# Kernel tuning notes

Measured on AMD Instinct MI355X. Metric: run time of the kernel, lower is better.

Reference implementation:

```python
import jax, jax.numpy as jnp
import numpy as np

B, S, D = 4, 2048, 1024
H, HD = 16, 64  # n_head, head_dim; H*HD == D

def setup_inputs() -> dict:
    key = jax.random.key(0)
    k1, k2, k3 = jax.random.split(key, 3)
    x = jax.random.normal(k1, (B, S, D), dtype=jnp.float32)
    # nn.Linear weights: stored [out, in]; init ~ U(-1/sqrt(in), 1/sqrt(in))
    w_attn = jax.random.uniform(k2, (3 * D, D), dtype=jnp.float32,
                                minval=-1.0, maxval=1.0) / jnp.sqrt(jnp.float32(D))
    w_proj = jax.random.uniform(k3, (D, D), dtype=jnp.float32,
                                minval=-1.0, maxval=1.0) / jnp.sqrt(jnp.float32(D))
    return {"x": x, "w_attn": w_attn, "w_proj": w_proj}

def reference(x, w_attn, w_proj):
    b, s, d = x.shape
    qkv = jnp.einsum('bsd,ed->bse', x, w_attn)              # [b, s, 3D]
    q, k, v = jnp.split(qkv, 3, axis=-1)
    q = q.reshape(b, s, H, HD).transpose(0, 2, 1, 3)        # [b, h, s, hd]
    k = k.reshape(b, s, H, HD).transpose(0, 2, 1, 3)
    v = v.reshape(b, s, H, HD).transpose(0, 2, 1, 3)
    scale = 1.0 / jnp.sqrt(jnp.float32(HD))
    scores = jnp.einsum('bhqd,bhkd->bhqk', q, k) * scale    # [b, h, s, s]
    causal = jnp.tril(jnp.ones((s, s), dtype=bool))
    scores = jnp.where(causal[None, None], scores, -jnp.inf)
    attn = jax.nn.softmax(scores, axis=-1)
    out = jnp.einsum('bhqk,bhkd->bhqd', attn, v)            # [b, h, s, hd]
    out = out.transpose(0, 2, 1, 3).reshape(b, s, d)
    return jnp.einsum('bsd,ed->bse', out, w_proj)
```

## Files before the change

### kernel.cpp

```cpp
#include <hip/hip_runtime.h>
#include <hip/hip_bf16.h>

#define NB   4
#define SEQ  2048
#define DMODEL 1024
#define NHEAD 16
#define HDIM 64
#define MROWS (NB * SEQ)
#define N_QKV (3 * DMODEL)

typedef __attribute__((ext_vector_type(8))) short bf16x8;
typedef __attribute__((ext_vector_type(4))) float f32x4;

#define MFMA16(a, b, c) __builtin_amdgcn_mfma_f32_16x16x32_bf16((a), (b), (c), 0, 0, 0)

__device__ inline bf16x8 load16(const __hip_bfloat16* p) {
    union { uint4 u; bf16x8 v; } t;
    t.u = *(const uint4*)p;
    return t.v;
}

__device__ inline ushort f2bf(float f) {
    union { float f; unsigned int u; } a;
    a.f = f;
    unsigned int r = a.u + 0x7FFFu + ((a.u >> 16) & 1u);
    return (ushort)(r >> 16);
}

__device__ inline unsigned int cvt_pk_bf16(float lo, float hi) {
    unsigned int r;
    asm("v_cvt_pk_bf16_f32 %0, %1, %2" : "=v"(r) : "v"(lo), "v"(hi));
    return r;
}

__device__ inline void gload_lds16(const __hip_bfloat16* g, __hip_bfloat16* l) {
    __builtin_amdgcn_global_load_lds(
        (const __attribute__((address_space(1))) unsigned int*)g,
        (__attribute__((address_space(3))) unsigned int*)l,
        16, 0, 0);
}

__global__ __launch_bounds__(256)
void cast_bf16_kernel(const float* __restrict__ in, ushort* __restrict__ out, int n,
                      int scale_n, float sc) {
    int idx = (blockIdx.x * 256 + threadIdx.x) * 4;
    if (idx + 3 < n) {
        float4 v = *(const float4*)(in + idx);
        float s = (idx < scale_n) ? sc : 1.0f;
        ushort4 o;
        o.x = f2bf(v.x * s);
        o.y = f2bf(v.y * s);
        o.z = f2bf(v.z * s);
        o.w = f2bf(v.w * s);
        *(ushort4*)(out + idx) = o;
    }
}

template<int MODE>
__global__ __launch_bounds__(256)
void gemm_bt(const __hip_bfloat16* __restrict__ A,
             const __hip_bfloat16* __restrict__ Bm,
             ushort* __restrict__ Cb,
             float* __restrict__ Cf,
             ushort* __restrict__ Vt,
             int M, int N, int K) {
    constexpr int BM = 128, BN = 128, BK = 32, LDT = 32;
    __shared__ __hip_bfloat16 As[BM * LDT];
    __shared__ __hip_bfloat16 Bs[BN * LDT];

    const int tid  = threadIdx.x;
    const int lane = tid & 63;
    const int wave = tid >> 6;
    const int wr = (wave >> 1) * 64;
    const int wc = (wave & 1) * 64;
    const int quad = lane >> 4;
    const int l16  = lane & 15;

    const int row0 = blockIdx.y * BM;
    const int col0 = blockIdx.x * BN;

    const int srow = lane >> 2;
    const int scol = (lane & 3) * 8;

    f32x4 acc[4][4];
#pragma unroll
    for (int i = 0; i < 4; i++)
#pragma unroll
        for (int j = 0; j < 4; j++) acc[i][j] = (f32x4)0.0f;

    for (int k0 = 0; k0 < K; k0 += BK) {
#pragma unroll
        for (int c = 0; c < 2; c++) {
            const int seg = wave * 2 + c;
            const int r = seg * 16 + srow;
            gload_lds16(A  + (size_t)(row0 + r) * K + k0 + scol, As + seg * 512);
            gload_lds16(Bm + (size_t)(col0 + r) * K + k0 + scol, Bs + seg * 512);
        }
        __syncthreads();

        bf16x8 af[4], bfr[4];
#pragma unroll
        for (int t = 0; t < 4; t++) {
            af[t]  = load16(&As[(wr + t * 16 + l16) * LDT + quad * 8]);
            bfr[t] = load16(&Bs[(wc + t * 16 + l16) * LDT + quad * 8]);
        }
#pragma unroll
        for (int i = 0; i < 4; i++)
#pragma unroll
            for (int j = 0; j < 4; j++)
                acc[i][j] = MFMA16(af[i], bfr[j], acc[i][j]);
        __syncthreads();
    }

    if constexpr (MODE == 2) {
        if (col0 >= 2 * DMODEL) {
            __shared__ ushort Ts[64 * 136];
            const int vcol0 = col0 - 2 * DMODEL;
            const int bb = row0 >> 11;
            const int row0m = row0 & 2047;
#pragma unroll
            for (int half = 0; half < 2; half++) {
                if ((wave & 1) == half) {
#pragma unroll
                    for (int i = 0; i < 4; i++)
#pragma unroll
                        for (int j = 0; j < 4; j++) {
                            int c = j * 16 + l16;
                            int rb = wr + i * 16 + quad * 4;
#pragma unroll
                            for (int r = 0; r < 4; r++)
                                Ts[c * 136 + rb + r] = f2bf(acc[i][j][r]);
                        }
                }
                __syncthreads();
                int col = tid >> 2, part = tid & 3;
                int hh = (vcol0 >> 6) + half;
                ushort* dp = Vt + (((size_t)(bb * NHEAD + hh)) * HDIM + col) * SEQ
                                + row0m + part * 32;
                const ushort* sp = &Ts[col * 136 + part * 32];
#pragma unroll
                for (int k = 0; k < 4; k++)
                    *(uint4*)(dp + k * 8) = *(const uint4*)(sp + k * 8);
                __syncthreads();
            }
            return;
        }
    }

    ushort* base = nullptr;
    int c0 = 0;
    if constexpr (MODE == 2) {
        base = Cb + ((col0 >= DMODEL) ? (size_t)MROWS * DMODEL : 0);
        c0 = col0 & (DMODEL - 1);
    }
#pragma unroll
    for (int i = 0; i < 4; i++) {
#pragma unroll
        for (int r = 0; r < 4; r++) {
            size_t grow = (size_t)(row0 + wr + i * 16 + quad * 4 + r);
#pragma unroll
            for (int j = 0; j < 4; j++) {
                float v = acc[i][j][r];
                if (MODE == 1) {
                    Cf[grow * N + col0 + wc + j * 16 + l16] = v;
                } else {
                    base[grow * DMODEL + c0 + wc + j * 16 + l16] = f2bf(v);
                }
            }
        }
    }
}

__global__ __launch_bounds__(256)
void attn_kernel(const ushort* __restrict__ Qb, const ushort* __restrict__ Kb,
                 const ushort* __restrict__ Vtb, ushort* __restrict__ O) {
    constexpr int LDP = 40;
    __shared__ __hip_bfloat16 Kc[2 * 32 * 64];
    __shared__ __hip_bfloat16 Vc[2 * 64 * 32];
    __shared__ ushort Pld[4 * 16 * LDP];

    const int tid  = threadIdx.x;
    const int wave = tid >> 6;
    const int lane = tid & 63;
    const int quad = lane >> 4;
    const int l16  = lane & 15;

    const int blk = (int)blockIdx.x;
    const int g   = 15 - (blk >> 6);
    const int bh  = (((blk >> 3) & 7) << 3) | (blk & 7);
    const int b = bh >> 4, h = bh & 15;
    const int p  = 4 * g + wave;
    const int q0 = p * 32;
    const int nc = p + 1;
    const int ncmax = 4 * g + 4;

    bf16x8 ones;
#pragma unroll
    for (int i = 0; i < 8; i++) ones[i] = (short)0x3F80;

    bf16x8 qf[2][2];
#pragma unroll
    for (int s = 0; s < 2; s++) {
        const __hip_bfloat16* qp = (const __hip_bfloat16*)Qb
            + ((size_t)b * SEQ + q0 + s * 16 + l16) * DMODEL + h * HDIM;
        qf[s][0] = load16(qp + quad * 8);
        qf[s][1] = load16(qp + 32 + quad * 8);
    }

    const __hip_bfloat16* kbase = (const __hip_bfloat16*)Kb + (size_t)b * SEQ * DMODEL + h * HDIM;
    const __hip_bfloat16* vbase = (const __hip_bfloat16*)Vtb + (size_t)bh * HDIM * SEQ;

    f32x4 oacc[2][4], lacc[2];
#pragma unroll
    for (int s = 0; s < 2; s++) {
        lacc[s] = (f32x4)0.0f;
#pragma unroll
        for (int t = 0; t < 4; t++) oacc[s][t] = (f32x4)0.0f;
    }

    ushort* myP = Pld + wave * (16 * LDP);

    auto stage = [&](int k0, int buf) {
        const int slot = wave * 64 + lane;
        const int key = slot >> 3;
        const int dsg = (slot & 7) ^ (key & 7);
        gload_lds16(kbase + (size_t)(k0 + key) * DMODEL + dsg * 8,
                    Kc + buf * 2048 + wave * 512);
        const int d  = slot >> 2;
        const int sg = slot & 3;
        gload_lds16(vbase + (size_t)d * SEQ + k0 + sg * 8,
                    Vc + buf * 2048 + wave * 512);
    };

    stage(0, 0);
    __syncthreads();

    for (int c = 0; c < ncmax; ++c) {
        const int cur = c & 1;
        if (c + 1 < ncmax) stage((c + 1) * 32, cur ^ 1);

        if (c < nc) {
            const int k0 = c * 32;
            const bool diag = (c == nc - 1);
            const __hip_bfloat16* Kb_l = Kc + cur * 2048;
            const __hip_bfloat16* Vb_l = Vc + cur * 2048;

            bf16x8 kb[2][2], vb[4];
#pragma unroll
            for (int t = 0; t < 2; t++) {
#pragma unroll
                for (int hf = 0; hf < 2; hf++)
                    kb[t][hf] = load16(&Kb_l[(t * 16 + l16) * 64
                                             + (((hf * 4 + quad) ^ (l16 & 7)) * 8)]);
            }
#pragma unroll
            for (int t = 0; t < 4; t++)
                vb[t] = load16(&Vb_l[(t * 16 + l16) * 32 + quad * 8]);

#pragma unroll
            for (int s = 0; s < 2; s++) {
                f32x4 z[2];
#pragma unroll
                for (int t = 0; t < 2; t++) {
                    f32x4 zz = (f32x4)0.0f;
                    zz = MFMA16(kb[t][0], qf[s][0], zz);
                    zz = MFMA16(kb[t][1], qf[s][1], zz);
                    z[t] = zz;
                }

#pragma unroll
                for (int t = 0; t < 2; t++) {
                    float e[4];
#pragma unroll
                    for (int r = 0; r < 4; r++) {
                        float sv = z[t][r];
                        if (diag) {
                            int key = k0 + t * 16 + quad * 4 + r;
                            int qq  = q0 + s * 16 + l16;
                            sv = (key <= qq) ? sv : -1e30f;
                        }
                        e[r] = exp2f(sv);
                    }
                    uint2 w;
                    w.x = cvt_pk_bf16(e[0], e[1]);
                    w.y = cvt_pk_bf16(e[2], e[3]);
                    *(uint2*)&myP[l16 * LDP + t * 16 + quad * 4] = w;
                }
                bf16x8 pa = load16((const __hip_bfloat16*)&myP[l16 * LDP + quad * 8]);

#pragma unroll
                for (int t = 0; t < 4; t++)
                    oacc[s][t] = MFMA16(pa, vb[t], oacc[s][t]);
                lacc[s] = MFMA16(pa, ones, lacc[s]);
            }
        }
        __syncthreads();
    }

#pragma unroll
    for (int s = 0; s < 2; s++) {
        float inv[4];
#pragma unroll
        for (int r = 0; r < 4; r++) inv[r] = 1.0f / lacc[s][r];
#pragma unroll
        for (int t = 0; t < 4; t++) {
#pragma unroll
            for (int r = 0; r < 4; r++) {
                float v = oacc[s][t][r] * inv[r];
                O[((size_t)b * SEQ + q0 + s * 16 + quad * 4 + r) * DMODEL
                  + h * HDIM + t * 16 + l16] = f2bf(v);
            }
        }
    }
}

extern "C" void kernel_launch(void* const* d_in, const int* in_sizes, int n_in,
                              void* d_out, int out_size, void* d_ws, size_t ws_size,
                              hipStream_t stream) {
    const float* x      = (const float*)d_in[0];
    const float* w_attn = (const float*)d_in[1];
    const float* w_proj = (const float*)d_in[2];
    float* out = (float*)d_out;

    ushort* ws   = (ushort*)d_ws;
    ushort* xb   = ws;
    ushort* wab  = xb  + (size_t)MROWS * DMODEL;
    ushort* wpb  = wab + (size_t)N_QKV * DMODEL;
    ushort* qkvb = wpb + (size_t)DMODEL * DMODEL;
    ushort* ob   = qkvb + (size_t)MROWS * N_QKV;

    ushort* qreg = qkvb;
    ushort* kreg = qkvb + (size_t)MROWS * DMODEL;
    ushort* vtreg = qkvb + 2 * (size_t)MROWS * DMODEL;

    const int n_x  = MROWS * DMODEL;
    const int n_wa = N_QKV * DMODEL;
    const int n_wp = DMODEL * DMODEL;

    const float qsc = 0.125f * 1.44269504f;

    cast_bf16_kernel<<<n_x / 1024, 256, 0, stream>>>(x, xb, n_x, 0, 1.0f);
    cast_bf16_kernel<<<n_wa / 1024, 256, 0, stream>>>(w_attn, wab, n_wa,
                                                      DMODEL * DMODEL, qsc);
    cast_bf16_kernel<<<n_wp / 1024, 256, 0, stream>>>(w_proj, wpb, n_wp, 0, 1.0f);

    gemm_bt<2><<<dim3(N_QKV / 128, MROWS / 128), 256, 0, stream>>>(
        (const __hip_bfloat16*)xb, (const __hip_bfloat16*)wab, qreg, nullptr, vtreg,
        MROWS, N_QKV, DMODEL);

    attn_kernel<<<1024, 256, 0, stream>>>(qreg, kreg, vtreg, ob);

    gemm_bt<1><<<dim3(DMODEL / 128, MROWS / 128), 256, 0, stream>>>(
        (const __hip_bfloat16*)ob, (const __hip_bfloat16*)wpb, nullptr, out, nullptr,
        MROWS, DMODEL, DMODEL);
}
```

Baseline: 281.5 us.

## Triple-buffer K/V tiles in attention with partial vmcnt waits

Moves the attention kernel's K/V staging from double to triple buffering, prefetching two chunks ahead. The full __syncthreads is replaced by s_waitcnt vmcnt(2) plus a raw barrier, so only the oldest chunk's loads must land before each iteration. Staging pointers are precomputed and advanced incrementally, and exp2f becomes the hardware exp2 builtin. This uses more LDS per block, and correctness now depends on the hand-written vmcnt counts matching the number of outstanding loads.

```diff
diff --git a/kernel.cpp b/kernel.cpp
--- a/kernel.cpp
+++ b/kernel.cpp
@@ -175,8 +175,8 @@
 void attn_kernel(const ushort* __restrict__ Qb, const ushort* __restrict__ Kb,
                  const ushort* __restrict__ Vtb, ushort* __restrict__ O) {
     constexpr int LDP = 40;
-    __shared__ __hip_bfloat16 Kc[2 * 32 * 64];
-    __shared__ __hip_bfloat16 Vc[2 * 64 * 32];
+    __shared__ __hip_bfloat16 Kc[3 * 32 * 64];
+    __shared__ __hip_bfloat16 Vc[3 * 64 * 32];
     __shared__ ushort Pld[4 * 16 * LDP];
 
     const int tid  = threadIdx.x;
@@ -220,24 +220,31 @@
 
     ushort* myP = Pld + wave * (16 * LDP);
 
-    auto stage = [&](int k0, int buf) {
-        const int slot = wave * 64 + lane;
-        const int key = slot >> 3;
-        const int dsg = (slot & 7) ^ (key & 7);
-        gload_lds16(kbase + (size_t)(k0 + key) * DMODEL + dsg * 8,
-                    Kc + buf * 2048 + wave * 512);
-        const int d  = slot >> 2;
-        const int sg = slot & 3;
-        gload_lds16(vbase + (size_t)d * SEQ + k0 + sg * 8,
-                    Vc + buf * 2048 + wave * 512);
+    const int slot = wave * 64 + lane;
+    const int skey = slot >> 3;
+    const int sdsg = (slot & 7) ^ (skey & 7);
+    const int svd  = slot >> 2;
+    const int svsg = slot & 3;
+    const __hip_bfloat16* kg = kbase + (size_t)skey * DMODEL + sdsg * 8;
+    const __hip_bfloat16* vg = vbase + (size_t)svd * SEQ + svsg * 8;
+
+    auto stage = [&](int buf) {
+        gload_lds16(kg, Kc + buf * 2048 + wave * 512);
+        gload_lds16(vg, Vc + buf * 2048 + wave * 512);
+        kg += 32 * DMODEL;
+        vg += 32;
     };
 
-    stage(0, 0);
-    __syncthreads();
+    stage(0);
+    stage(1);
+    asm volatile("s_waitcnt vmcnt(2)" ::: "memory");
+    __builtin_amdgcn_s_barrier();
+    asm volatile("" ::: "memory");
 
     for (int c = 0; c < ncmax; ++c) {
-        const int cur = c & 1;
-        if (c + 1 < ncmax) stage((c + 1) * 32, cur ^ 1);
+        const int cur = c % 3;
+        const bool more = (c + 2 < ncmax);
+        if (more) stage((c + 2) % 3);
 
         if (c < nc) {
             const int k0 = c * 32;
@@ -279,7 +286,7 @@
                             int qq  = q0 + s * 16 + l16;
                             sv = (key <= qq) ? sv : -1e30f;
                         }
-                        e[r] = exp2f(sv);
+                        e[r] = __builtin_amdgcn_exp2f(sv);
                     }
                     uint2 w;
                     w.x = cvt_pk_bf16(e[0], e[1]);
@@ -294,7 +301,11 @@
                 lacc[s] = MFMA16(pa, ones, lacc[s]);
             }
         }
-        __syncthreads();
+
+        if (more) asm volatile("s_waitcnt vmcnt(2)" ::: "memory");
+        else      asm volatile("s_waitcnt vmcnt(0)" ::: "memory");
+        __builtin_amdgcn_s_barrier();
+        asm volatile("" ::: "memory");
     }
 
 #pragma unroll
```

Result: no change. 281.5 us (+0.0%).
